# Optimization experiments

Hardware: AMD Instinct MI355X
Metric: run time of the kernel (lower is better)

## Reference

```python
import jax, jax.numpy as jnp
import numpy as np

N_NODES = 2000
LN_EPS = 1e-5
NEG_SLOPE = 0.2  # PyG GATConv default


def _gat(xg, W, b, a_src, a_dst, src, dst):
    # xg: [G, N, Fin]; single-head GATConv, add_self_loops=False
    h = xg @ W                      # [G, N, H]
    es = h @ a_src                  # [G, N]
    ed = h @ a_dst                  # [G, N]
    e = jax.nn.leaky_relu(es[:, src] + ed[:, dst], NEG_SLOPE)  # [G, E]

    def seg_softmax(e_g):
        m = jax.ops.segment_max(e_g, dst, num_segments=N_NODES)
        ex = jnp.exp(e_g - m[dst])
        s = jax.ops.segment_sum(ex, dst, num_segments=N_NODES)
        return ex / (s[dst] + 1e-16)

    alpha = jax.vmap(seg_softmax)(e)            # [G, E]
    msg = alpha[..., None] * h[:, src]          # [G, E, H]
    agg = jax.vmap(lambda m_: jax.ops.segment_sum(m_, dst, num_segments=N_NODES))(msg)
    return agg + b                              # [G, N, H]


def _gcn_layer(x, W, b, a_src, a_dst, src, dst):
    # x: [B, N, T, F] -- faithfully replicate original permute + raw reshape
    B, N, T, F = x.shape
    x_in = jnp.transpose(x, (0, 2, 1, 3)).reshape(B * T, N, F)
    out = _gat(x_in, W, b, a_src, a_dst, src, dst)          # [B*T, N, H]
    out = jax.nn.gelu(out.reshape(B, T, N, -1), approximate=False)
    # original does .reshape(B, N, T, -1) on a [B,T,N,H]-contiguous tensor
    return out.reshape(B, N, T, -1)


def _lstm(x, Wih, Whh, bih, bhh):
    # x: [BN, T, Fin]; torch LSTM gate order i,f,g,o
    BN, T, _ = x.shape
    H = Whh.shape[1]
    xz = x @ Wih.T + (bih + bhh)                # [BN, T, 4H]

    def step(carry, z_t):
        h, c = carry
        z = z_t + h @ Whh.T
        i, f, g, o = jnp.split(z, 4, axis=-1)
        c = jax.nn.sigmoid(f) * c + jax.nn.sigmoid(i) * jnp.tanh(g)
        h = jax.nn.sigmoid(o) * jnp.tanh(c)
        return (h, c), h

    init = (jnp.zeros((BN, H), x.dtype), jnp.zeros((BN, H), x.dtype))
    _, hs = jax.lax.scan(step, init, jnp.swapaxes(xz, 0, 1))
    return jnp.swapaxes(hs, 0, 1)               # [BN, T, H]


def setup_inputs() -> dict:
    key = jax.random.key(0)
    ks = jax.random.split(key, 20)
    B, N, T, NX, H, PL, NY, E = 2, N_NODES, 24, 8, 64, 12, 1, 32000
    p = {}
    p["x"] = jax.random.normal(ks[0], (B, N, T, NX), jnp.float32)
    p["edge_src"] = jax.random.randint(ks[1], (E,), 0, N, jnp.int32)
    p["edge_dst"] = jax.random.randint(ks[2], (E,), 0, N, jnp.int32)
    p["fc_W"] = jax.random.normal(ks[3], (NX, H), jnp.float32) / np.sqrt(NX)
    p["fc_b"] = jnp.zeros((H,), jnp.float32)
    for i, tag in enumerate(["g1", "g2"]):
        p[f"{tag}_W"] = jax.random.normal(ks[4 + 4 * i], (H, H), jnp.float32) / np.sqrt(H)
        p[f"{tag}_b"] = jnp.zeros((H,), jnp.float32)
        p[f"{tag}_asrc"] = jax.random.normal(ks[5 + 4 * i], (H,), jnp.float32) / np.sqrt(H)
        p[f"{tag}_adst"] = jax.random.normal(ks[6 + 4 * i], (H,), jnp.float32) / np.sqrt(H)
    p["lstm_Wih"] = jax.random.normal(ks[12], (4 * H, H), jnp.float32) / np.sqrt(H)
    p["lstm_Whh"] = jax.random.normal(ks[13], (4 * H, H), jnp.float32) / np.sqrt(H)
    p["lstm_bih"] = jnp.zeros((4 * H,), jnp.float32)
    p["lstm_bhh"] = jnp.zeros((4 * H,), jnp.float32)
    p["ln_g"] = jnp.ones((H,), jnp.float32)
    p["ln_b"] = jnp.zeros((H,), jnp.float32)
    p["dense_W"] = jax.random.normal(ks[14], (H, PL * NY), jnp.float32) / np.sqrt(H)
    p["dense_b"] = jnp.zeros((PL * NY,), jnp.float32)
    return p


def reference(x, edge_src, edge_dst, fc_W, fc_b,
              g1_W, g1_b, g1_asrc, g1_adst,
              g2_W, g2_b, g2_asrc, g2_adst,
              lstm_Wih, lstm_Whh, lstm_bih, lstm_bhh,
              ln_g, ln_b, dense_W, dense_b):
    B, N, T, _ = x.shape
    PRED_LEN, NY = 12, 1
    x_h = x @ fc_W + fc_b                                        # [B,N,T,H]
    g1 = _gcn_layer(x_h, g1_W, g1_b, g1_asrc, g1_adst, edge_src, edge_dst)
    g2 = _gcn_layer(g1, g2_W, g2_b, g2_asrc, g2_adst, edge_src, edge_dst)
    H = g2.shape[-1]
    lout = _lstm(g2.reshape(B * N, T, -1), lstm_Wih, lstm_Whh, lstm_bih, lstm_bhh)
    lout = lout.reshape(B, N, T, H)
    mu = jnp.mean(lout, axis=-1, keepdims=True)
    var = jnp.mean(jnp.square(lout - mu), axis=-1, keepdims=True)
    h = (lout - mu) / jnp.sqrt(var + LN_EPS) * ln_g + ln_b
    out = h[:, :, -1:, :] @ dense_W + dense_b                    # [B,N,1,PL*NY]
    return out.reshape(B, N, PRED_LEN, NY)
```

## Files before the change

kernel.cpp:

```cpp
#include <hip/hip_runtime.h>
#include <hip/hip_bf16.h>
#include <math.h>

#define B_   2
#define N_   2000
#define T_   24
#define NX_  8
#define H_   64
#define G_   (B_*T_)
#define E_   32000
#define BN_  (B_*N_)
#define TH_  (T_*H_)
#define NTH_ (N_*T_*H_)
#define GNH_ (G_*N_*H_)
#define NPARAM_ 43340
#define NPARAM_PAD_ 43392
#define LSTM_PAD 72
#define DEGCAP 64

using bf16 = __hip_bfloat16;
typedef short bf16x8 __attribute__((ext_vector_type(8)));
typedef float f32x4  __attribute__((ext_vector_type(4)));

__device__ __forceinline__ float uasf(unsigned u){ return __uint_as_float(u); }
__device__ __forceinline__ float wave_sum(float v){
  #pragma unroll
  for (int o = 32; o > 0; o >>= 1) v += __shfl_xor(v, o, 64);
  return v;
}
__device__ __forceinline__ float fastrcp(float x){ return __builtin_amdgcn_rcpf(x); }
__device__ __forceinline__ float sigf(float x){ return fastrcp(1.f + __expf(-x)); }
__device__ __forceinline__ float tanhfast(float x){ return 1.f - 2.f*fastrcp(1.f + __expf(2.f*x)); }
__device__ __forceinline__ float gelu_exact(float x){ return 0.5f*x*(1.f + erff(x*0.70710678118654752f)); }
__device__ __forceinline__ unsigned f2bf_rtn(float f){
  unsigned u = __float_as_uint(f);
  u += 0x7fffu + ((u >> 16) & 1u);
  return u >> 16;
}
__device__ __forceinline__ bf16x8 pack8(float4 a, float4 b){
  bf16x8 v;
  v[0]=(short)f2bf_rtn(a.x); v[1]=(short)f2bf_rtn(a.y);
  v[2]=(short)f2bf_rtn(a.z); v[3]=(short)f2bf_rtn(a.w);
  v[4]=(short)f2bf_rtn(b.x); v[5]=(short)f2bf_rtn(b.y);
  v[6]=(short)f2bf_rtn(b.z); v[7]=(short)f2bf_rtn(b.w);
  return v;
}

struct ConvArgs {
  const void* src[18];
  int off[19];
};
__global__ __launch_bounds__(256) void prep_kernel(
    ConvArgs a, const unsigned* __restrict__ xw,
    float* __restrict__ dst, int* __restrict__ flag,
    int* __restrict__ cnt_g,
    float* __restrict__ wc, float* __restrict__ bc){
  __shared__ int scnt;
  int tid = threadIdx.x;
  if (tid == 0) scnt = 0;
  __syncthreads();
  int c = 0;
  for (int i = tid; i < 4096; i += 256){
    unsigned e = (xw[i] >> 7) & 0xffu;
    if (e >= 100u && e <= 140u) c++;
  }
  atomicAdd(&scnt, c);
  __syncthreads();
  int isbf = (scnt > 3276) ? 1 : 0;
  int bid = blockIdx.x;

  if (bid < 170){
    if (bid == 0 && tid == 0) *flag = isbf;
    int i = bid*256 + tid;
    if (i < NPARAM_){
      int seg = 0;
      while (i >= a.off[seg+1]) seg++;
      int j = i - a.off[seg];
      float v;
      if (isbf) v = uasf(((unsigned)((const unsigned short*)a.src[seg])[j]) << 16);
      else      v = ((const float*)a.src[seg])[j];
      dst[i] = v;
    }
  } else if (bid == 170){
    for (int i = tid; i < N_; i += 256) cnt_g[i] = 0;
  } else {
    const void* pfcW = a.src[0];
    const void* pfcb = a.src[1];
    const void* pg1W = a.src[2];
    #pragma unroll
    for (int half = 0; half < 2; ++half){
      int t2 = half*256 + tid;
      int i = t2 >> 6, n = t2 & 63;
      float s = 0.f;
      #pragma unroll
      for (int k = 0; k < 64; ++k){
        float fa = isbf ? uasf(((unsigned)((const unsigned short*)pfcW)[i*64+k]) << 16)
                        : ((const float*)pfcW)[i*64+k];
        float fb = isbf ? uasf(((unsigned)((const unsigned short*)pg1W)[k*64+n]) << 16)
                        : ((const float*)pg1W)[k*64+n];
        s = fmaf(fa, fb, s);
      }
      wc[i*64 + n] = s;
    }
    if (tid < 64){
      float b = 0.f;
      #pragma unroll
      for (int k = 0; k < 64; ++k){
        float fa = isbf ? uasf(((unsigned)((const unsigned short*)pfcb)[k]) << 16)
                        : ((const float*)pfcb)[k];
        float fb = isbf ? uasf(((unsigned)((const unsigned short*)pg1W)[k*64+tid]) << 16)
                        : ((const float*)pg1W)[k*64+tid];
        b = fmaf(fa, fb, b);
      }
      bc[tid] = b;
    }
  }
}

__global__ __launch_bounds__(256) void gat_h1_fused_kernel(
    const void* __restrict__ xraw, const int* __restrict__ flag,
    const int* __restrict__ esrc, const int* __restrict__ edst,
    int* __restrict__ cnt_g, int* __restrict__ slot,
    const float* __restrict__ wc, const float* __restrict__ bc,
    const float* __restrict__ asrc, const float* __restrict__ adst,
    unsigned short* __restrict__ hbuf, float* __restrict__ es, float* __restrict__ ed){
  if (blockIdx.x < 125){
    int e = blockIdx.x*256 + threadIdx.x;
    int d = edst[e];
    int pos = atomicAdd(&cnt_g[d], 1);
    if (pos < DEGCAP) slot[(d << 6) + pos] = esrc[e];
  }
  int lane = threadIdx.x & 63, wave = threadIdx.x >> 6;
  int q = lane >> 4, c = lane & 15;
  int isbf = *flag;
  bf16x8 Bf[4];
  #pragma unroll
  for (int nt = 0; nt < 4; ++nt){
    bf16x8 v;
    #pragma unroll
    for (int j = 0; j < 8; ++j)
      v[j] = (q == 0) ? (short)f2bf_rtn(wc[j*64 + nt*16 + c]) : (short)0;
    Bf[nt] = v;
  }
  float bcv[4];
  #pragma unroll
  for (int nt = 0; nt < 4; ++nt) bcv[nt] = bc[nt*16 + c];
  float aS[4], aD[4];
  #pragma unroll
  for (int nt = 0; nt < 4; ++nt){ aS[nt] = asrc[nt*16+c]; aD[nt] = adst[nt*16+c]; }

  int w = blockIdx.x*4 + wave;
  #pragma unroll
  for (int it = 0; it < 2; ++it){
    int tile = w*2 + it;
    int p0 = tile*16;
    int g  = p0 / N_, n0 = p0 - g*N_;
    int bb = g / T_,  tt = g - bb*T_;
    bf16x8 A0;
    #pragma unroll
    for (int j = 0; j < 8; ++j) A0[j] = 0;
    if (q == 0){
      size_t rowelt = ((size_t)(bb*N_ + n0 + c)*T_ + tt)*NX_;
      if (isbf){
        A0 = *(const bf16x8*)((const unsigned short*)xraw + rowelt);
      } else {
        const float4* xr4 = (const float4*)((const float*)xraw + rowelt);
        A0 = pack8(xr4[0], xr4[1]);
      }
    }
    f32x4 acc[4];
    #pragma unroll
    for (int nt = 0; nt < 4; ++nt){ acc[nt][0]=bcv[nt]; acc[nt][1]=bcv[nt]; acc[nt][2]=bcv[nt]; acc[nt][3]=bcv[nt]; }
    #pragma unroll
    for (int nt = 0; nt < 4; ++nt) acc[nt] = __builtin_amdgcn_mfma_f32_16x16x32_bf16(A0, Bf[nt], acc[nt], 0, 0, 0);

    #pragma unroll
    for (int nt = 0; nt < 4; ++nt){
      #pragma unroll
      for (int r = 0; r < 4; ++r)
        hbuf[(size_t)(p0 + q*4 + r)*H_ + nt*16 + c] = (unsigned short)f2bf_rtn(acc[nt][r]);
    }
    #pragma unroll
    for (int r = 0; r < 4; ++r){
      float e1 = acc[0][r]*aS[0] + acc[1][r]*aS[1] + acc[2][r]*aS[2] + acc[3][r]*aS[3];
      float e2 = acc[0][r]*aD[0] + acc[1][r]*aD[1] + acc[2][r]*aD[2] + acc[3][r]*aD[3];
      #pragma unroll
      for (int o = 8; o > 0; o >>= 1){
        e1 += __shfl_xor(e1, o, 64);
        e2 += __shfl_xor(e2, o, 64);
      }
      if (c == 0){
        es[p0 + q*4 + r] = e1;
        ed[p0 + q*4 + r] = e2;
      }
    }
  }
}

__global__ __launch_bounds__(256) void gat_h2_mfma_kernel(
    const float* __restrict__ xin, const float* __restrict__ W,
    const float* __restrict__ asrc, const float* __restrict__ adst,
    unsigned short* __restrict__ hbuf, float* __restrict__ es, float* __restrict__ ed){
  int lane = threadIdx.x & 63, wave = threadIdx.x >> 6;
  int q = lane >> 4, c = lane & 15;
  bf16x8 Bf[4][2];
  #pragma unroll
  for (int nt = 0; nt < 4; ++nt){
    #pragma unroll
    for (int ks = 0; ks < 2; ++ks){
      bf16x8 v;
      #pragma unroll
      for (int j = 0; j < 8; ++j)
        v[j] = (short)f2bf_rtn(W[(ks*32 + q*8 + j)*H_ + nt*16 + c]);
      Bf[nt][ks] = v;
    }
  }
  float aS[4], aD[4];
  #pragma unroll
  for (int nt = 0; nt < 4; ++nt){ aS[nt] = asrc[nt*16+c]; aD[nt] = adst[nt*16+c]; }

  int w = blockIdx.x*4 + wave;
  #pragma unroll
  for (int it = 0; it < 2; ++it){
    int tile = w*2 + it;
    int p0 = tile*16;
    int p  = p0 + c;
    int g = p / N_, n = p - g*N_;
    int bb = g / T_, t = g - bb*T_;
    const float4* xr4 = (const float4*)(xin + (size_t)bb*NTH_ + (size_t)n*TH_ + (size_t)t*H_);
    float4 x0 = xr4[q*2],     x1 = xr4[q*2 + 1];
    float4 x2 = xr4[8 + q*2], x3 = xr4[8 + q*2 + 1];
    bf16x8 A0 = pack8(x0, x1);
    bf16x8 A1 = pack8(x2, x3);

    f32x4 acc[4];
    #pragma unroll
    for (int nt = 0; nt < 4; ++nt){ acc[nt][0]=0.f; acc[nt][1]=0.f; acc[nt][2]=0.f; acc[nt][3]=0.f; }
    #pragma unroll
    for (int nt = 0; nt < 4; ++nt) acc[nt] = __builtin_amdgcn_mfma_f32_16x16x32_bf16(A0, Bf[nt][0], acc[nt], 0, 0, 0);
    #pragma unroll
    for (int nt = 0; nt < 4; ++nt) acc[nt] = __builtin_amdgcn_mfma_f32_16x16x32_bf16(A1, Bf[nt][1], acc[nt], 0, 0, 0);

    #pragma unroll
    for (int nt = 0; nt < 4; ++nt){
      #pragma unroll
      for (int r = 0; r < 4; ++r)
        hbuf[(size_t)(p0 + q*4 + r)*H_ + nt*16 + c] = (unsigned short)f2bf_rtn(acc[nt][r]);
    }
    #pragma unroll
    for (int r = 0; r < 4; ++r){
      float e1 = acc[0][r]*aS[0] + acc[1][r]*aS[1] + acc[2][r]*aS[2] + acc[3][r]*aS[3];
      float e2 = acc[0][r]*aD[0] + acc[1][r]*aD[1] + acc[2][r]*aD[2] + acc[3][r]*aD[3];
      #pragma unroll
      for (int o = 8; o > 0; o >>= 1){
        e1 += __shfl_xor(e1, o, 64);
        e2 += __shfl_xor(e2, o, 64);
      }
      if (c == 0){
        es[p0 + q*4 + r] = e1;
        ed[p0 + q*4 + r] = e2;
      }
    }
  }
}

__global__ __launch_bounds__(256) void gat_agg_kernel(
    const unsigned short* __restrict__ hbuf, const float* __restrict__ es, const float* __restrict__ ed,
    const int* __restrict__ cnt_g, const int* __restrict__ slot,
    const float* __restrict__ bias, float* __restrict__ gout){
  int lane = threadIdx.x & 63, wave = threadIdx.x >> 6;
  int qd = lane >> 4, ln = lane & 15;
  int gd = (blockIdx.x*4 + wave)*4 + qd;
  int g = gd / N_, d = gd - g*N_;
  int start = d << 6;
  int deg = min(cnt_g[d], DEGCAP);
  const float* esg = es + (size_t)g*N_;
  float edv = ed[(size_t)g*N_ + d];
  const char* hg = (const char*)(hbuf + (size_t)g*N_*H_);
  unsigned lanoff = ((unsigned)ln) << 3;
  int hbase = qd << 4;
  int dm = deg;
  dm = max(dm, __shfl_xor(dm, 16, 64));
  dm = max(dm, __shfl_xor(dm, 32, 64));
  int NC = (dm + 15) >> 4;

  int svk[4]; float sck[4];
  #pragma unroll
  for (int k = 0; k < 4; ++k){ svk[k] = 0; sck[k] = -1e30f; }
  #pragma unroll
  for (int k = 0; k < 4; ++k){
    int i = k*16 + ln;
    if (k < NC && i < deg) svk[k] = slot[start + i];
  }
  #pragma unroll
  for (int k = 0; k < 4; ++k){
    int i = k*16 + ln;
    if (k < NC && i < deg){
      float e = esg[svk[k]] + edv;
      sck[k] = e > 0.f ? e : 0.2f*e;
    }
  }
  float m = fmaxf(fmaxf(sck[0], sck[1]), fmaxf(sck[2], sck[3]));
  #pragma unroll
  for (int o = 8; o > 0; o >>= 1) m = fmaxf(m, __shfl_xor(m, o, 64));
  float exk[4]; float ssum = 0.f;
  #pragma unroll
  for (int k = 0; k < 4; ++k){
    int i = k*16 + ln;
    float e = (k < NC && i < deg) ? __expf(sck[k] - m) : 0.f;
    exk[k] = e; ssum += e;
  }
  #pragma unroll
  for (int o = 8; o > 0; o >>= 1) ssum += __shfl_xor(ssum, o, 64);
  float inv = fastrcp(ssum + 1e-16f);
  unsigned pwk[4];
  #pragma unroll
  for (int k = 0; k < 4; ++k)
    pwk[k] = (f2bf_rtn(exk[k]*inv) << 16) | (unsigned)svk[k];

  float a0 = 0.f, a1 = 0.f, a2 = 0.f, a3 = 0.f;
  for (int k = 0; k < NC; ++k){
    unsigned pw = pwk[k];
    int myrem = deg - k*16;
    int remw = dm - k*16; if (remw > 16) remw = 16;
    for (int j0 = 0; j0 < remw; j0 += 8){
      unsigned wv[8]; float aa[8]; unsigned off[8];
      #pragma unroll
      for (int u = 0; u < 8; ++u){
        int j = j0 + u;
        wv[u] = (unsigned)__shfl((int)pw, hbase + j, 64);
        aa[u] = (j < myrem) ? uasf(wv[u] & 0xffff0000u) : 0.f;
        off[u] = ((wv[u] & 0xffffu) << 7) + lanoff;
      }
      uint2 hv[8];
      #pragma unroll
      for (int u = 0; u < 8; ++u)
        hv[u] = *(const uint2*)(hg + off[u]);
      #pragma unroll
      for (int u = 0; u < 8; ++u){
        a0 = fmaf(aa[u], uasf(hv[u].x << 16), a0);
        a1 = fmaf(aa[u], uasf(hv[u].x & 0xffff0000u), a1);
        a2 = fmaf(aa[u], uasf(hv[u].y << 16), a2);
        a3 = fmaf(aa[u], uasf(hv[u].y & 0xffff0000u), a3);
      }
    }
  }
  float4 bv = ((const float4*)bias)[ln];
  float4 o4;
  o4.x = gelu_exact(a0 + bv.x);
  o4.y = gelu_exact(a1 + bv.y);
  o4.z = gelu_exact(a2 + bv.z);
  o4.w = gelu_exact(a3 + bv.w);
  ((float4*)(gout + (size_t)gd*H_))[ln] = o4;
}

__global__ __launch_bounds__(256) void lstm_final_kernel(
    const float* __restrict__ xin,
    const float* __restrict__ Wih,
    const float* __restrict__ Whh,
    const float* __restrict__ bih, const float* __restrict__ bhh,
    const float* __restrict__ lng, const float* __restrict__ lnb,
    const float* __restrict__ dW, const float* __restrict__ db,
    const int* __restrict__ flag, void* __restrict__ outv){
  __shared__ __align__(16) unsigned short Hlds[16*LSTM_PAD];
  __shared__ float smH[16][68];
  int tid = threadIdx.x;
  int lane = tid & 63, wave = tid >> 6;
  int q = lane >> 4, c = lane & 15;
  int s0 = blockIdx.x * 16;

  bf16x8 Bf[4][4];
  #pragma unroll
  for (int g = 0; g < 4; ++g){
    int n = g*64 + wave*16 + c;
    #pragma unroll
    for (int ks = 0; ks < 4; ++ks){
      const float* srcp = (ks < 2) ? (Whh + (size_t)n*64 + ks*32 + q*8)
                                   : (Wih + (size_t)n*64 + (ks-2)*32 + q*8);
      float4 a = ((const float4*)srcp)[0];
      float4 b = ((const float4*)srcp)[1];
      Bf[g][ks] = pack8(a, b);
    }
  }
  float bsum[4];
  #pragma unroll
  for (int g = 0; g < 4; ++g){
    int n = g*64 + wave*16 + c;
    bsum[g] = bih[n] + bhh[n];
  }
  for (int i = tid; i < 16*LSTM_PAD; i += 256) Hlds[i] = 0;
  float cst[4] = {0.f, 0.f, 0.f, 0.f};
  __syncthreads();

  for (int t = 0; t < T_; ++t){
    const float4* xr4 = (const float4*)(xin + ((size_t)(s0 + c)*T_ + t)*64);
    float4 x0 = xr4[q*2],     x1 = xr4[q*2 + 1];
    float4 x2 = xr4[8 + q*2], x3 = xr4[8 + q*2 + 1];
    bf16x8 Ax0 = pack8(x0, x1);
    bf16x8 Ax1 = pack8(x2, x3);
    const bf16x8* hrow = (const bf16x8*)(Hlds + c*LSTM_PAD);
    bf16x8 Ah0 = hrow[q];
    bf16x8 Ah1 = hrow[4 + q];

    f32x4 acc[4];
    #pragma unroll
    for (int g = 0; g < 4; ++g){ acc[g][0]=bsum[g]; acc[g][1]=bsum[g]; acc[g][2]=bsum[g]; acc[g][3]=bsum[g]; }
    #pragma unroll
    for (int g = 0; g < 4; ++g) acc[g] = __builtin_amdgcn_mfma_f32_16x16x32_bf16(Ah0, Bf[g][0], acc[g], 0, 0, 0);
    #pragma unroll
    for (int g = 0; g < 4; ++g) acc[g] = __builtin_amdgcn_mfma_f32_16x16x32_bf16(Ah1, Bf[g][1], acc[g], 0, 0, 0);
    #pragma unroll
    for (int g = 0; g < 4; ++g) acc[g] = __builtin_amdgcn_mfma_f32_16x16x32_bf16(Ax0, Bf[g][2], acc[g], 0, 0, 0);
    #pragma unroll
    for (int g = 0; g < 4; ++g) acc[g] = __builtin_amdgcn_mfma_f32_16x16x32_bf16(Ax1, Bf[g][3], acc[g], 0, 0, 0);

    float hv[4];
    #pragma unroll
    for (int r = 0; r < 4; ++r){
      float zi = acc[0][r], zf = acc[1][r], zg = acc[2][r], zo = acc[3][r];
      cst[r] = sigf(zf)*cst[r] + sigf(zi)*tanhfast(zg);
      hv[r] = sigf(zo)*tanhfast(cst[r]);
    }
    if (t == T_-1){
      #pragma unroll
      for (int r = 0; r < 4; ++r)
        smH[q*4 + r][wave*16 + c] = hv[r];
    } else {
      __syncthreads();
      #pragma unroll
      for (int r = 0; r < 4; ++r)
        Hlds[(q*4 + r)*LSTM_PAD + wave*16 + c] = (unsigned short)f2bf_rtn(hv[r]);
      __syncthreads();
    }
  }
  __syncthreads();

  int isbf = *flag;
  #pragma unroll
  for (int si = 0; si < 4; ++si){
    int s = wave*4 + si;
    float h = smH[s][lane];
    float mu = wave_sum(h) * (1.f/64.f);
    float dev = h - mu;
    float var = wave_sum(dev*dev) * (1.f/64.f);
    float hn = dev * rsqrtf(var + 1e-5f) * lng[lane] + lnb[lane];
    smH[s][lane] = hn;
    if (lane < 12){
      float o = db[lane];
      #pragma unroll
      for (int k = 0; k < 64; ++k) o = fmaf(smH[s][k], dW[k*12 + lane], o);
      size_t oi = (size_t)(s0 + s)*12 + lane;
      if (isbf) ((unsigned short*)outv)[oi] = (unsigned short)f2bf_rtn(o);
      else      ((float*)outv)[oi] = o;
    }
  }
}

extern "C" void kernel_launch(void* const* d_in, const int* in_sizes, int n_in,
                              void* d_out, int out_size, void* d_ws, size_t ws_size,
                              hipStream_t stream) {
  const int* esrc = (const int*)d_in[1];
  const int* edst = (const int*)d_in[2];

  static const int sizes[18] = {512, 64, 4096, 64, 64, 64, 4096, 64, 64, 64,
                                16384, 16384, 256, 256, 64, 64, 768, 12};
  static const int srcidx[18] = {3, 4, 5, 6, 7, 8, 9, 10, 11, 12,
                                 13, 14, 15, 16, 17, 18, 19, 20};
  ConvArgs ca;
  {
    int acc = 0;
    for (int i = 0; i < 18; ++i){ ca.src[i] = d_in[srcidx[i]]; ca.off[i] = acc; acc += sizes[i]; }
    ca.off[18] = acc;
  }

  float* P     = (float*)d_ws;
  float* bufA  = P + NPARAM_PAD_;
  float* bufB  = bufA + (size_t)GNH_;
  float* esb   = bufB + (size_t)GNH_;
  float* edb   = esb  + (size_t)G_*N_;
  int*   cnt_g = (int*)(edb + (size_t)G_*N_);
  int*   slot  = cnt_g + N_;
  int*   flag  = slot + N_*DEGCAP;
  float* wcb   = (float*)(flag + 1);
  unsigned short* hbuf = (unsigned short*)bufB;

  const float* pg1b = P + 4672;
  const float* pg1as= P + 4736;
  const float* pg1ad= P + 4800;
  const float* pg2W = P + 4864;
  const float* pg2b = P + 8960;
  const float* pg2as= P + 9024;
  const float* pg2ad= P + 9088;
  const float* pWih = P + 9152;
  const float* pWhh = P + 25536;
  const float* pbih = P + 41920;
  const float* pbhh = P + 42176;
  const float* plng = P + 42432;
  const float* plnb = P + 42496;
  const float* pdW  = P + 42560;
  const float* pdb  = P + 43328;

  prep_kernel<<<172, 256, 0, stream>>>(ca, (const unsigned*)d_in[0],
                                       P, flag, cnt_g, wcb, wcb + 512);

  gat_h1_fused_kernel<<<750, 256, 0, stream>>>(d_in[0], flag, esrc, edst, cnt_g, slot,
                                               wcb, wcb + 512, pg1as, pg1ad, hbuf, esb, edb);
  gat_agg_kernel<<<6000, 256, 0, stream>>>(hbuf, esb, edb, cnt_g, slot, pg1b, bufA);

  gat_h2_mfma_kernel<<<750, 256, 0, stream>>>(bufA, pg2W, pg2as, pg2ad, hbuf, esb, edb);
  gat_agg_kernel<<<6000, 256, 0, stream>>>(hbuf, esb, edb, cnt_g, slot, pg2b, bufA);

  lstm_final_kernel<<<250, 256, 0, stream>>>(bufA, pWih, pWhh, pbih, pbhh,
                                             plng, plnb, pdW, pdb, flag, d_out);
}
```

Measured before the change: 233.2 us.

## Store GAT outputs as bf16 and double-buffer LSTM hidden state in LDS

```diff
diff --git a/kernel.cpp b/kernel.cpp
--- a/kernel.cpp
+++ b/kernel.cpp
@@ -198,7 +198,7 @@
 }
 
 __global__ __launch_bounds__(256) void gat_h2_mfma_kernel(
-    const float* __restrict__ xin, const float* __restrict__ W,
+    const unsigned short* __restrict__ xinb, const float* __restrict__ W,
     const float* __restrict__ asrc, const float* __restrict__ adst,
     unsigned short* __restrict__ hbuf, float* __restrict__ es, float* __restrict__ ed){
   int lane = threadIdx.x & 63, wave = threadIdx.x >> 6;
@@ -227,11 +227,9 @@
     int p  = p0 + c;
     int g = p / N_, n = p - g*N_;
     int bb = g / T_, t = g - bb*T_;
-    const float4* xr4 = (const float4*)(xin + (size_t)bb*NTH_ + (size_t)n*TH_ + (size_t)t*H_);
-    float4 x0 = xr4[q*2],     x1 = xr4[q*2 + 1];
-    float4 x2 = xr4[8 + q*2], x3 = xr4[8 + q*2 + 1];
-    bf16x8 A0 = pack8(x0, x1);
-    bf16x8 A1 = pack8(x2, x3);
+    const unsigned short* xr = xinb + (size_t)bb*NTH_ + (size_t)n*TH_ + (size_t)t*H_;
+    bf16x8 A0 = *(const bf16x8*)(xr + q*8);
+    bf16x8 A1 = *(const bf16x8*)(xr + 32 + q*8);
 
     f32x4 acc[4];
     #pragma unroll
@@ -267,7 +265,7 @@
 __global__ __launch_bounds__(256) void gat_agg_kernel(
     const unsigned short* __restrict__ hbuf, const float* __restrict__ es, const float* __restrict__ ed,
     const int* __restrict__ cnt_g, const int* __restrict__ slot,
-    const float* __restrict__ bias, float* __restrict__ gout){
+    const float* __restrict__ bias, unsigned short* __restrict__ goutb){
   int lane = threadIdx.x & 63, wave = threadIdx.x >> 6;
   int qd = lane >> 4, ln = lane & 15;
   int gd = (blockIdx.x*4 + wave)*4 + qd;
@@ -346,23 +344,21 @@
     }
   }
   float4 bv = ((const float4*)bias)[ln];
-  float4 o4;
-  o4.x = gelu_exact(a0 + bv.x);
-  o4.y = gelu_exact(a1 + bv.y);
-  o4.z = gelu_exact(a2 + bv.z);
-  o4.w = gelu_exact(a3 + bv.w);
-  ((float4*)(gout + (size_t)gd*H_))[ln] = o4;
+  uint2 ov;
+  ov.x = f2bf_rtn(gelu_exact(a0 + bv.x)) | (f2bf_rtn(gelu_exact(a1 + bv.y)) << 16);
+  ov.y = f2bf_rtn(gelu_exact(a2 + bv.z)) | (f2bf_rtn(gelu_exact(a3 + bv.w)) << 16);
+  ((uint2*)(goutb + (size_t)gd*H_))[ln] = ov;
 }
 
 __global__ __launch_bounds__(256) void lstm_final_kernel(
-    const float* __restrict__ xin,
+    const unsigned short* __restrict__ xinb,
     const float* __restrict__ Wih,
     const float* __restrict__ Whh,
     const float* __restrict__ bih, const float* __restrict__ bhh,
     const float* __restrict__ lng, const float* __restrict__ lnb,
     const float* __restrict__ dW, const float* __restrict__ db,
     const int* __restrict__ flag, void* __restrict__ outv){
-  __shared__ __align__(16) unsigned short Hlds[16*LSTM_PAD];
+  __shared__ __align__(16) unsigned short Hlds[2][16*LSTM_PAD];
   __shared__ float smH[16][68];
   int tid = threadIdx.x;
   int lane = tid & 63, wave = tid >> 6;
@@ -388,17 +384,16 @@
     int n = g*64 + wave*16 + c;
     bsum[g] = bih[n] + bhh[n];
   }
-  for (int i = tid; i < 16*LSTM_PAD; i += 256) Hlds[i] = 0;
+  for (int i = tid; i < 16*LSTM_PAD; i += 256) Hlds[0][i] = 0;
   float cst[4] = {0.f, 0.f, 0.f, 0.f};
   __syncthreads();
 
+  int buf = 0;
   for (int t = 0; t < T_; ++t){
-    const float4* xr4 = (const float4*)(xin + ((size_t)(s0 + c)*T_ + t)*64);
-    float4 x0 = xr4[q*2],     x1 = xr4[q*2 + 1];
-    float4 x2 = xr4[8 + q*2], x3 = xr4[8 + q*2 + 1];
-    bf16x8 Ax0 = pack8(x0, x1);
-    bf16x8 Ax1 = pack8(x2, x3);
-    const bf16x8* hrow = (const bf16x8*)(Hlds + c*LSTM_PAD);
+    const unsigned short* xr = xinb + ((size_t)(s0 + c)*T_ + t)*64;
+    bf16x8 Ax0 = *(const bf16x8*)(xr + q*8);
+    bf16x8 Ax1 = *(const bf16x8*)(xr + 32 + q*8);
+    const bf16x8* hrow = (const bf16x8*)(Hlds[buf] + c*LSTM_PAD);
     bf16x8 Ah0 = hrow[q];
     bf16x8 Ah1 = hrow[4 + q];
 
@@ -426,11 +421,11 @@
       for (int r = 0; r < 4; ++r)
         smH[q*4 + r][wave*16 + c] = hv[r];
     } else {
+      #pragma unroll
+      for (int r = 0; r < 4; ++r)
+        Hlds[buf^1][(q*4 + r)*LSTM_PAD + wave*16 + c] = (unsigned short)f2bf_rtn(hv[r]);
       __syncthreads();
-      #pragma unroll
-      for (int r = 0; r < 4; ++r)
-        Hlds[(q*4 + r)*LSTM_PAD + wave*16 + c] = (unsigned short)f2bf_rtn(hv[r]);
-      __syncthreads();
+      buf ^= 1;
     }
   }
   __syncthreads();
@@ -475,14 +470,15 @@
 
   float* P     = (float*)d_ws;
   float* bufA  = P + NPARAM_PAD_;
-  float* bufB  = bufA + (size_t)GNH_;
-  float* esb   = bufB + (size_t)GNH_;
+  float* bufB  = bufA + (size_t)GNH_/2 + 64;
+  float* esb   = bufB + (size_t)GNH_/2 + 64;
   float* edb   = esb  + (size_t)G_*N_;
   int*   cnt_g = (int*)(edb + (size_t)G_*N_);
   int*   slot  = cnt_g + N_;
   int*   flag  = slot + N_*DEGCAP;
   float* wcb   = (float*)(flag + 1);
-  unsigned short* hbuf = (unsigned short*)bufB;
+  unsigned short* goutb = (unsigned short*)bufA;
+  unsigned short* hbuf  = (unsigned short*)bufB;
 
   const float* pg1b = P + 4672;
   const float* pg1as= P + 4736;
@@ -505,11 +501,11 @@
 
   gat_h1_fused_kernel<<<750, 256, 0, stream>>>(d_in[0], flag, esrc, edst, cnt_g, slot,
                                                wcb, wcb + 512, pg1as, pg1ad, hbuf, esb, edb);
-  gat_agg_kernel<<<6000, 256, 0, stream>>>(hbuf, esb, edb, cnt_g, slot, pg1b, bufA);
-
-  gat_h2_mfma_kernel<<<750, 256, 0, stream>>>(bufA, pg2W, pg2as, pg2ad, hbuf, esb, edb);
-  gat_agg_kernel<<<6000, 256, 0, stream>>>(hbuf, esb, edb, cnt_g, slot, pg2b, bufA);
-
-  lstm_final_kernel<<<250, 256, 0, stream>>>(bufA, pWih, pWhh, pbih, pbhh,
+  gat_agg_kernel<<<6000, 256, 0, stream>>>(hbuf, esb, edb, cnt_g, slot, pg1b, goutb);
+
+  gat_h2_mfma_kernel<<<750, 256, 0, stream>>>(goutb, pg2W, pg2as, pg2ad, hbuf, esb, edb);
+  gat_agg_kernel<<<6000, 256, 0, stream>>>(hbuf, esb, edb, cnt_g, slot, pg2b, goutb);
+
+  lstm_final_kernel<<<250, 256, 0, stream>>>(goutb, pWih, pWhh, pbih, pbhh,
                                              plng, plnb, pdW, pdb, flag, d_out);
 }
```

New measurement: 226.6 us. -2.8%, faster.
